# Optimization experiments

Measured on AMD Instinct MI355X. Metric: run time of the kernel, lower is better.

The kernel has to match this reference:

```python
import jax, jax.numpy as jnp
import numpy as np

B, S, H, T = 64, 512, 768, 3


def setup_inputs() -> dict:
    key = jax.random.key(0)
    ks = jax.random.split(key, 8)
    hidden = jax.random.normal(ks[0], (B, S, H), dtype=jnp.float32)
    labels = jax.random.randint(ks[1], (B, S), 0, T, dtype=jnp.int32)
    # variable-length attention mask; torchcrf requires mask[:, 0] all on
    lengths = jax.random.randint(ks[2], (B,), S // 4, S + 1, dtype=jnp.int32)
    mask = (jnp.arange(S)[None, :] < lengths[:, None]).astype(jnp.int32)
    W = jax.random.normal(ks[3], (H, T), dtype=jnp.float32) * 0.02
    b = jax.random.normal(ks[4], (T,), dtype=jnp.float32) * 0.02
    transitions = jax.random.normal(ks[5], (T, T), dtype=jnp.float32) * 0.1
    start_trans = jax.random.normal(ks[6], (T,), dtype=jnp.float32) * 0.1
    end_trans = jax.random.normal(ks[7], (T,), dtype=jnp.float32) * 0.1
    return {"hidden": hidden, "labels": labels, "mask": mask, "W": W, "b": b,
            "transitions": transitions, "start_trans": start_trans, "end_trans": end_trans}


def _crf_nll(emissions, tags, mask, trans, start, end):
    # emissions: (B,S,T) float; tags/mask: (B,S) int. Returns sum NLL (scalar).
    mask_f = mask.astype(emissions.dtype)
    bidx = jnp.arange(emissions.shape[0])
    # --- numerator: score of the given tag path ---
    first_tag = tags[:, 0]
    num = start[first_tag] + emissions[bidx, 0, first_tag]
    prev, cur = tags[:, :-1], tags[:, 1:]
    step = trans[prev, cur] + jnp.take_along_axis(emissions[:, 1:], cur[..., None], axis=2)[..., 0]
    num = num + jnp.sum(step * mask_f[:, 1:], axis=1)
    lengths = jnp.sum(mask, axis=1)
    last_tag = jnp.take_along_axis(tags, (lengths - 1)[:, None], axis=1)[:, 0]
    num = num + end[last_tag]
    # --- denominator: log-partition via forward algorithm (lax.scan) ---
    alpha0 = start[None, :] + emissions[:, 0]  # (B,T)
    def fwd_step(alpha, inp):
        e, m = inp  # e: (B,T), m: (B,)
        nxt = jax.scipy.special.logsumexp(alpha[:, :, None] + trans[None] + e[:, None, :], axis=1)
        return jnp.where(m[:, None] > 0, nxt, alpha), None
    emis_t = jnp.swapaxes(emissions[:, 1:], 0, 1)  # (S-1,B,T)
    mask_t = jnp.swapaxes(mask[:, 1:], 0, 1)       # (S-1,B)
    alpha, _ = jax.lax.scan(fwd_step, alpha0, (emis_t, mask_t))
    logZ = jax.scipy.special.logsumexp(alpha + end[None, :], axis=1)
    return jnp.sum(logZ - num)


def reference(hidden, labels, mask, W, b, transitions, start_trans, end_trans):
    # classifier: Linear + ReLU -> emissions (B,S,T)
    emissions = jax.nn.relu(jnp.einsum("bsh,ht->bst", hidden, W) + b)
    negloglike = _crf_nll(emissions, labels, mask, transitions, start_trans, end_trans)
    return emissions, negloglike
```

## Files before the change

kernel.cpp:

```cpp
#include <hip/hip_runtime.h>
#include <math.h>

#define NB 64
#define NS 512
#define NH 768
#define NT 3
#define EMIS_N (NB * NS * NT)
#define NEGINF (-1e30f)
#define PSTRIDE 12
#define BPB 16
#define NBLK 1024

typedef float floatx4 __attribute__((ext_vector_type(4)));

__device__ __forceinline__ float lse3(float a, float b, float c) {
    float m = fmaxf(fmaxf(a, b), c);
    return m + __logf(__expf(a - m) + __expf(b - m) + __expf(c - m));
}

__global__ __launch_bounds__(512) void emis_crf_kernel(
    const float* __restrict__ hidden,
    const int*   __restrict__ labels,
    const int*   __restrict__ mask,
    const float* __restrict__ W,
    const float* __restrict__ bias,
    const float* __restrict__ trans,
    const float* __restrict__ startv,
    const float* __restrict__ endv,
    float* __restrict__ out,
    float* __restrict__ ws)
{
    __shared__ float sP[8][12];
    __shared__ alignas(16) float wlds[NH * NT];

    const int tid  = threadIdx.x;
    const int lane = tid & 63;
    const int wv   = tid >> 6;
    const int wid  = blockIdx.x * 8 + wv;
    const int sub  = lane & 15;
    const int rsel = lane >> 4;
    const int row  = wid * 4 + rsel;
    const int b    = row >> 9;
    const int p    = row & (NS - 1);

    if (blockIdx.x == 0 && tid == 0) out[EMIS_N] = 0.0f;

    {
        const float4* Wv = reinterpret_cast<const float4*>(W);
        float4* Lv = reinterpret_cast<float4*>(wlds);
        Lv[tid] = Wv[tid];
        if (tid < 64) Lv[512 + tid] = Wv[512 + tid];
    }

    const int* lrow = labels + b * NS;
    const int* mrow = mask   + b * NS;
    int mk = 0, mk1 = 0, labc = 0, labp = 0;
    if (sub == 0) {
        mk   = mrow[p];
        mk1  = (p < NS - 1) ? mrow[p + 1] : 0;
        labc = lrow[p];
        labp = lrow[p - (p > 0 ? 1 : 0)];
    }

    __syncthreads();

    const float* hrow = hidden + (size_t)row * NH;
    float a0 = 0.f, a1 = 0.f, a2 = 0.f;
    #pragma unroll
    for (int it = 0; it < 12; ++it) {
        const int h0 = it * 64 + sub * 4;
        const floatx4 x = __builtin_nontemporal_load(
                              reinterpret_cast<const floatx4*>(hrow + h0));
        const float4 q0 = *reinterpret_cast<const float4*>(wlds + h0 * 3);
        const float4 q1 = *reinterpret_cast<const float4*>(wlds + h0 * 3 + 4);
        const float4 q2 = *reinterpret_cast<const float4*>(wlds + h0 * 3 + 8);
        a0 = fmaf(x.x, q0.x, a0); a1 = fmaf(x.x, q0.y, a1); a2 = fmaf(x.x, q0.z, a2);
        a0 = fmaf(x.y, q0.w, a0); a1 = fmaf(x.y, q1.x, a1); a2 = fmaf(x.y, q1.y, a2);
        a0 = fmaf(x.z, q1.z, a0); a1 = fmaf(x.z, q1.w, a1); a2 = fmaf(x.z, q2.x, a2);
        a0 = fmaf(x.w, q2.y, a0); a1 = fmaf(x.w, q2.z, a1); a2 = fmaf(x.w, q2.w, a2);
    }
    #pragma unroll
    for (int d = 8; d; d >>= 1) {
        a0 += __shfl_xor(a0, d);
        a1 += __shfl_xor(a1, d);
        a2 += __shfl_xor(a2, d);
    }

    const float e0 = fmaxf(a0 + bias[0], 0.f);
    const float e1 = fmaxf(a1 + bias[1], 0.f);
    const float e2 = fmaxf(a2 + bias[2], 0.f);

    if (sub < 3) out[row * NT + sub] = (sub == 0) ? e0 : (sub == 1) ? e1 : e2;

    float term = 0.f;
    if (sub == 0) {
        const float esel = (labc == 0) ? e0 : (labc == 1) ? e1 : e2;
        if (p == 0) {
            term = startv[labc] + esel;
        } else if (mk) {
            term = trans[labp * 3 + labc] + esel;
        }
        if (mk && mk1 == 0) term += endv[labc];
    }

    const int il = (lane < 9) ? (lane / 3) : 0;
    const int jl = (lane < 9) ? (lane % 3) : 0;
    const float tc0 = trans[jl], tc1 = trans[3 + jl], tc2 = trans[6 + jl];
    float Pv = (il == jl) ? 0.f : NEGINF;

    const int pbase = p & ~3;
    #pragma unroll
    for (int k = 0; k < 4; ++k) {
        const int src = k << 4;
        const float ee0 = __shfl(e0, src);
        const float ee1 = __shfl(e1, src);
        const float ee2 = __shfl(e2, src);
        const int   mm  = __shfl(mk, src);
        const float Pi0 = __shfl(Pv, il * 3 + 0);
        const float Pi1 = __shfl(Pv, il * 3 + 1);
        const float Pi2 = __shfl(Pv, il * 3 + 2);
        const float ej  = (jl == 0) ? ee0 : (jl == 1) ? ee1 : ee2;
        const float q   = lse3(Pi0 + tc0, Pi1 + tc1, Pi2 + tc2) + ej;
        const bool act  = ((pbase + k) >= 1) && (mm != 0);
        Pv = act ? q : Pv;
    }

    const float np = __shfl(term, 0) + __shfl(term, 16) +
                     __shfl(term, 32) + __shfl(term, 48);

    if (lane < 9)  sP[wv][lane] = Pv;
    if (lane == 0) sP[wv][9]    = np;
    __syncthreads();
    if (wv != 0) return;

    float Pb = (lane < 9) ? sP[0][lane] : 0.f;
    #pragma unroll
    for (int k = 1; k < 8; ++k) {
        const float Pi0 = __shfl(Pb, il * 3 + 0);
        const float Pi1 = __shfl(Pb, il * 3 + 1);
        const float Pi2 = __shfl(Pb, il * 3 + 2);
        const float q = lse3(Pi0 + sP[k][jl],
                             Pi1 + sP[k][3 + jl],
                             Pi2 + sP[k][6 + jl]);
        Pb = (lane < 9) ? q : Pb;
    }
    float* wp = ws + blockIdx.x * PSTRIDE;
    if (lane < 9)  wp[lane] = Pb;
    if (lane == 0) wp[9] = sP[0][9] + sP[1][9] + sP[2][9] + sP[3][9] +
                           sP[4][9] + sP[5][9] + sP[6][9] + sP[7][9];
}

__global__ __launch_bounds__(64) void crf_combine(
    const float* __restrict__ emis,
    const float* __restrict__ startv,
    const float* __restrict__ endv,
    const float* __restrict__ ws,
    float* __restrict__ nll)
{
    const int b    = blockIdx.x;
    const int lane = threadIdx.x;

    float P[9] = {0.f, NEGINF, NEGINF, NEGINF, 0.f, NEGINF, NEGINF, NEGINF, 0.f};
    float np = 0.f;
    if (lane < BPB) {
        const float* pa = ws + ((size_t)b * BPB + lane) * PSTRIDE;
        #pragma unroll
        for (int i = 0; i < 9; ++i) P[i] = pa[i];
        np = pa[9];
    }

    #pragma unroll
    for (int d = 1; d < BPB; d <<= 1) {
        float Q[9];
        #pragma unroll
        for (int i = 0; i < 9; ++i) Q[i] = __shfl_down(P[i], d);
        const bool valid = (lane + d) < BPB;
        float R[9];
        #pragma unroll
        for (int i = 0; i < 3; ++i)
            #pragma unroll
            for (int j = 0; j < 3; ++j)
                R[i * 3 + j] = lse3(P[i * 3 + 0] + Q[0 + j],
                                    P[i * 3 + 1] + Q[3 + j],
                                    P[i * 3 + 2] + Q[6 + j]);
        #pragma unroll
        for (int i = 0; i < 9; ++i) P[i] = valid ? R[i] : P[i];
    }

    #pragma unroll
    for (int d = 32; d; d >>= 1) np += __shfl_xor(np, d);

    if (lane == 0) {
        const float* erow = emis + (size_t)b * NS * NT;
        const float a0 = startv[0] + erow[0];
        const float a1 = startv[1] + erow[1];
        const float a2 = startv[2] + erow[2];
        const float f0 = lse3(a0 + P[0], a1 + P[3], a2 + P[6]);
        const float f1 = lse3(a0 + P[1], a1 + P[4], a2 + P[7]);
        const float f2 = lse3(a0 + P[2], a1 + P[5], a2 + P[8]);
        const float logZ = lse3(f0 + endv[0], f1 + endv[1], f2 + endv[2]);
        atomicAdd(nll, logZ - np);
    }
}

extern "C" void kernel_launch(void* const* d_in, const int* in_sizes, int n_in,
                              void* d_out, int out_size, void* d_ws, size_t ws_size,
                              hipStream_t stream) {
    const float* hidden = (const float*)d_in[0];
    const int*   labels = (const int*)  d_in[1];
    const int*   maskp  = (const int*)  d_in[2];
    const float* W      = (const float*)d_in[3];
    const float* bias   = (const float*)d_in[4];
    const float* trans  = (const float*)d_in[5];
    const float* startv = (const float*)d_in[6];
    const float* endv   = (const float*)d_in[7];
    float* out = (float*)d_out;
    float* ws  = (float*)d_ws;

    emis_crf_kernel<<<NBLK, 512, 0, stream>>>(hidden, labels, maskp, W, bias,
                                              trans, startv, endv, out, ws);
    crf_combine<<<NB, 64, 0, stream>>>(out, startv, endv, ws, out + EMIS_N);
}
```

Measured before the change: 26.03 us.

## Halve grid with two groups per wave and move block-level CRF combine to combine kernel

The main kernel now launches half as many blocks. Each wave processes two 4-row groups, writing per-group 3x3 transfer matrices directly to workspace instead of reducing them across waves through shared memory and a second barrier. The combine kernel then reduces 128 partials per batch: each lane first merges two partials, then runs a full 64-lane shuffle tree. This removes the in-block serial reduction and halves the W-to-LDS staging, at the cost of more workspace traffic and a longer combine scan.

```diff
diff --git a/kernel.cpp b/kernel.cpp
--- a/kernel.cpp
+++ b/kernel.cpp
@@ -8,8 +8,8 @@
 #define EMIS_N (NB * NS * NT)
 #define NEGINF (-1e30f)
 #define PSTRIDE 12
-#define BPB 16
-#define NBLK 1024
+#define GPB 128
+#define NBLK 512
 
 typedef float floatx4 __attribute__((ext_vector_type(4)));
 
@@ -30,18 +30,13 @@
     float* __restrict__ out,
     float* __restrict__ ws)
 {
-    __shared__ float sP[8][12];
     __shared__ alignas(16) float wlds[NH * NT];
 
     const int tid  = threadIdx.x;
     const int lane = tid & 63;
     const int wv   = tid >> 6;
-    const int wid  = blockIdx.x * 8 + wv;
     const int sub  = lane & 15;
     const int rsel = lane >> 4;
-    const int row  = wid * 4 + rsel;
-    const int b    = row >> 9;
-    const int p    = row & (NS - 1);
 
     if (blockIdx.x == 0 && tid == 0) out[EMIS_N] = 0.0f;
 
@@ -51,103 +46,93 @@
         Lv[tid] = Wv[tid];
         if (tid < 64) Lv[512 + tid] = Wv[512 + tid];
     }
-
-    const int* lrow = labels + b * NS;
-    const int* mrow = mask   + b * NS;
-    int mk = 0, mk1 = 0, labc = 0, labp = 0;
-    if (sub == 0) {
-        mk   = mrow[p];
-        mk1  = (p < NS - 1) ? mrow[p + 1] : 0;
-        labc = lrow[p];
-        labp = lrow[p - (p > 0 ? 1 : 0)];
-    }
-
     __syncthreads();
-
-    const float* hrow = hidden + (size_t)row * NH;
-    float a0 = 0.f, a1 = 0.f, a2 = 0.f;
-    #pragma unroll
-    for (int it = 0; it < 12; ++it) {
-        const int h0 = it * 64 + sub * 4;
-        const floatx4 x = __builtin_nontemporal_load(
-                              reinterpret_cast<const floatx4*>(hrow + h0));
-        const float4 q0 = *reinterpret_cast<const float4*>(wlds + h0 * 3);
-        const float4 q1 = *reinterpret_cast<const float4*>(wlds + h0 * 3 + 4);
-        const float4 q2 = *reinterpret_cast<const float4*>(wlds + h0 * 3 + 8);
-        a0 = fmaf(x.x, q0.x, a0); a1 = fmaf(x.x, q0.y, a1); a2 = fmaf(x.x, q0.z, a2);
-        a0 = fmaf(x.y, q0.w, a0); a1 = fmaf(x.y, q1.x, a1); a2 = fmaf(x.y, q1.y, a2);
-        a0 = fmaf(x.z, q1.z, a0); a1 = fmaf(x.z, q1.w, a1); a2 = fmaf(x.z, q2.x, a2);
-        a0 = fmaf(x.w, q2.y, a0); a1 = fmaf(x.w, q2.z, a1); a2 = fmaf(x.w, q2.w, a2);
-    }
-    #pragma unroll
-    for (int d = 8; d; d >>= 1) {
-        a0 += __shfl_xor(a0, d);
-        a1 += __shfl_xor(a1, d);
-        a2 += __shfl_xor(a2, d);
-    }
-
-    const float e0 = fmaxf(a0 + bias[0], 0.f);
-    const float e1 = fmaxf(a1 + bias[1], 0.f);
-    const float e2 = fmaxf(a2 + bias[2], 0.f);
-
-    if (sub < 3) out[row * NT + sub] = (sub == 0) ? e0 : (sub == 1) ? e1 : e2;
-
-    float term = 0.f;
-    if (sub == 0) {
-        const float esel = (labc == 0) ? e0 : (labc == 1) ? e1 : e2;
-        if (p == 0) {
-            term = startv[labc] + esel;
-        } else if (mk) {
-            term = trans[labp * 3 + labc] + esel;
-        }
-        if (mk && mk1 == 0) term += endv[labc];
-    }
 
     const int il = (lane < 9) ? (lane / 3) : 0;
     const int jl = (lane < 9) ? (lane % 3) : 0;
     const float tc0 = trans[jl], tc1 = trans[3 + jl], tc2 = trans[6 + jl];
-    float Pv = (il == jl) ? 0.f : NEGINF;
-
-    const int pbase = p & ~3;
-    #pragma unroll
-    for (int k = 0; k < 4; ++k) {
-        const int src = k << 4;
-        const float ee0 = __shfl(e0, src);
-        const float ee1 = __shfl(e1, src);
-        const float ee2 = __shfl(e2, src);
-        const int   mm  = __shfl(mk, src);
-        const float Pi0 = __shfl(Pv, il * 3 + 0);
-        const float Pi1 = __shfl(Pv, il * 3 + 1);
-        const float Pi2 = __shfl(Pv, il * 3 + 2);
-        const float ej  = (jl == 0) ? ee0 : (jl == 1) ? ee1 : ee2;
-        const float q   = lse3(Pi0 + tc0, Pi1 + tc1, Pi2 + tc2) + ej;
-        const bool act  = ((pbase + k) >= 1) && (mm != 0);
-        Pv = act ? q : Pv;
-    }
-
-    const float np = __shfl(term, 0) + __shfl(term, 16) +
-                     __shfl(term, 32) + __shfl(term, 48);
-
-    if (lane < 9)  sP[wv][lane] = Pv;
-    if (lane == 0) sP[wv][9]    = np;
-    __syncthreads();
-    if (wv != 0) return;
-
-    float Pb = (lane < 9) ? sP[0][lane] : 0.f;
-    #pragma unroll
-    for (int k = 1; k < 8; ++k) {
-        const float Pi0 = __shfl(Pb, il * 3 + 0);
-        const float Pi1 = __shfl(Pb, il * 3 + 1);
-        const float Pi2 = __shfl(Pb, il * 3 + 2);
-        const float q = lse3(Pi0 + sP[k][jl],
-                             Pi1 + sP[k][3 + jl],
-                             Pi2 + sP[k][6 + jl]);
-        Pb = (lane < 9) ? q : Pb;
-    }
-    float* wp = ws + blockIdx.x * PSTRIDE;
-    if (lane < 9)  wp[lane] = Pb;
-    if (lane == 0) wp[9] = sP[0][9] + sP[1][9] + sP[2][9] + sP[3][9] +
-                           sP[4][9] + sP[5][9] + sP[6][9] + sP[7][9];
+
+    #pragma unroll 1
+    for (int t = 0; t < 2; ++t) {
+        const int g    = (blockIdx.x * 8 + wv) + t * 4096;
+        const int row  = g * 4 + rsel;
+        const int b    = row >> 9;
+        const int p    = row & (NS - 1);
+
+        const int* lrow = labels + b * NS;
+        const int* mrow = mask   + b * NS;
+        int mk = 0, mk1 = 0, labc = 0, labp = 0;
+        if (sub == 0) {
+            mk   = mrow[p];
+            mk1  = (p < NS - 1) ? mrow[p + 1] : 0;
+            labc = lrow[p];
+            labp = lrow[p - (p > 0 ? 1 : 0)];
+        }
+
+        const float* hrow = hidden + (size_t)row * NH;
+        float a0 = 0.f, a1 = 0.f, a2 = 0.f;
+        #pragma unroll
+        for (int it = 0; it < 12; ++it) {
+            const int h0 = it * 64 + sub * 4;
+            const floatx4 x = __builtin_nontemporal_load(
+                                  reinterpret_cast<const floatx4*>(hrow + h0));
+            const float4 q0 = *reinterpret_cast<const float4*>(wlds + h0 * 3);
+            const float4 q1 = *reinterpret_cast<const float4*>(wlds + h0 * 3 + 4);
+            const float4 q2 = *reinterpret_cast<const float4*>(wlds + h0 * 3 + 8);
+            a0 = fmaf(x.x, q0.x, a0); a1 = fmaf(x.x, q0.y, a1); a2 = fmaf(x.x, q0.z, a2);
+            a0 = fmaf(x.y, q0.w, a0); a1 = fmaf(x.y, q1.x, a1); a2 = fmaf(x.y, q1.y, a2);
+            a0 = fmaf(x.z, q1.z, a0); a1 = fmaf(x.z, q1.w, a1); a2 = fmaf(x.z, q2.x, a2);
+            a0 = fmaf(x.w, q2.y, a0); a1 = fmaf(x.w, q2.z, a1); a2 = fmaf(x.w, q2.w, a2);
+        }
+        #pragma unroll
+        for (int d = 8; d; d >>= 1) {
+            a0 += __shfl_xor(a0, d);
+            a1 += __shfl_xor(a1, d);
+            a2 += __shfl_xor(a2, d);
+        }
+
+        const float e0 = fmaxf(a0 + bias[0], 0.f);
+        const float e1 = fmaxf(a1 + bias[1], 0.f);
+        const float e2 = fmaxf(a2 + bias[2], 0.f);
+
+        if (sub < 3) out[row * NT + sub] = (sub == 0) ? e0 : (sub == 1) ? e1 : e2;
+
+        float term = 0.f;
+        if (sub == 0) {
+            const float esel = (labc == 0) ? e0 : (labc == 1) ? e1 : e2;
+            if (p == 0) {
+                term = startv[labc] + esel;
+            } else if (mk) {
+                term = trans[labp * 3 + labc] + esel;
+            }
+            if (mk && mk1 == 0) term += endv[labc];
+        }
+
+        float Pv = (il == jl) ? 0.f : NEGINF;
+        const int pbase = (g * 4) & (NS - 1);
+        #pragma unroll
+        for (int k = 0; k < 4; ++k) {
+            const int src = k << 4;
+            const float ee0 = __shfl(e0, src);
+            const float ee1 = __shfl(e1, src);
+            const float ee2 = __shfl(e2, src);
+            const int   mm  = __shfl(mk, src);
+            const float Pi0 = __shfl(Pv, il * 3 + 0);
+            const float Pi1 = __shfl(Pv, il * 3 + 1);
+            const float Pi2 = __shfl(Pv, il * 3 + 2);
+            const float ej  = (jl == 0) ? ee0 : (jl == 1) ? ee1 : ee2;
+            const float q   = lse3(Pi0 + tc0, Pi1 + tc1, Pi2 + tc2) + ej;
+            const bool act  = ((pbase + k) >= 1) && (mm != 0);
+            Pv = act ? q : Pv;
+        }
+
+        const float np = __shfl(term, 0) + __shfl(term, 16) +
+                         __shfl(term, 32) + __shfl(term, 48);
+
+        float* wp = ws + (size_t)g * PSTRIDE;
+        if (lane < 9)  wp[lane] = Pv;
+        if (lane == 0) wp[9] = np;
+    }
 }
 
 __global__ __launch_bounds__(64) void crf_combine(
@@ -160,21 +145,31 @@
     const int b    = blockIdx.x;
     const int lane = threadIdx.x;
 
-    float P[9] = {0.f, NEGINF, NEGINF, NEGINF, 0.f, NEGINF, NEGINF, NEGINF, 0.f};
-    float np = 0.f;
-    if (lane < BPB) {
-        const float* pa = ws + ((size_t)b * BPB + lane) * PSTRIDE;
-        #pragma unroll
-        for (int i = 0; i < 9; ++i) P[i] = pa[i];
-        np = pa[9];
-    }
-
-    #pragma unroll
-    for (int d = 1; d < BPB; d <<= 1) {
+    const float* base = ws + (size_t)b * GPB * PSTRIDE;
+    const float* pa = base + (2 * lane)     * PSTRIDE;
+    const float* pb = base + (2 * lane + 1) * PSTRIDE;
+    float A[9], Bm[9];
+    #pragma unroll
+    for (int i = 0; i < 9; ++i) A[i]  = pa[i];
+    #pragma unroll
+    for (int i = 0; i < 9; ++i) Bm[i] = pb[i];
+    float np = pa[9] + pb[9];
+
+    float P[9];
+    #pragma unroll
+    for (int i = 0; i < 3; ++i)
+        #pragma unroll
+        for (int j = 0; j < 3; ++j)
+            P[i * 3 + j] = lse3(A[i * 3 + 0] + Bm[0 + j],
+                                A[i * 3 + 1] + Bm[3 + j],
+                                A[i * 3 + 2] + Bm[6 + j]);
+
+    #pragma unroll
+    for (int d = 1; d < 64; d <<= 1) {
         float Q[9];
         #pragma unroll
         for (int i = 0; i < 9; ++i) Q[i] = __shfl_down(P[i], d);
-        const bool valid = (lane + d) < BPB;
+        const bool valid = (lane + d) < 64;
         float R[9];
         #pragma unroll
         for (int i = 0; i < 3; ++i)
```

Measured after the change: 30.90 us. 1.19x slower.
